# Kernel tuning notes

Measured on AMD Instinct MI355X. Metric: run time of the kernel, lower is better.

The kernel has to match this reference:

```python
import jax, jax.numpy as jnp
import numpy as np

N_NODES = 50000
N_EDGES = 800000
F_IN = 512
HID = 128
OUT = 20


def setup_inputs() -> dict:
    key = jax.random.key(0)
    k1, k2, k3, k4, k5 = jax.random.split(key, 5)
    x = jax.random.normal(k1, (N_NODES, F_IN), dtype=jnp.float32)
    edge_index = jax.random.randint(k2, (2, N_EDGES), 0, N_NODES, dtype=jnp.int64)
    edge_weight = jax.random.uniform(k3, (N_EDGES,), dtype=jnp.float32)
    W1 = jax.random.normal(k4, (F_IN, HID), dtype=jnp.float32) * 0.05
    b1 = jnp.zeros((HID,), dtype=jnp.float32)
    W2 = jax.random.normal(k5, (HID, OUT), dtype=jnp.float32) * 0.05
    b2 = jnp.zeros((OUT,), dtype=jnp.float32)
    return {"x": x, "edge_index": edge_index, "edge_weight": edge_weight,
            "W1": W1, "b1": b1, "W2": W2, "b2": b2}


def _gcn_norm(edge_index, edge_weight, num_nodes):
    # PyG gcn_norm: add self-loops (weight 1), symmetric D^-1/2 (A+I) D^-1/2
    row, col = edge_index[0], edge_index[1]
    loop = jnp.arange(num_nodes, dtype=row.dtype)
    row = jnp.concatenate([row, loop])
    col = jnp.concatenate([col, loop])
    w = jnp.concatenate([edge_weight, jnp.ones((num_nodes,), edge_weight.dtype)])
    deg = jax.ops.segment_sum(w, col, num_segments=num_nodes)
    dinv = jnp.where(deg > 0, jax.lax.rsqrt(deg), 0.0)
    norm = dinv[row] * w * dinv[col]
    return row, col, norm


def _gcn_conv(x, W, b, row, col, norm, num_nodes):
    # linear first (in >= out), then gather-scale-scatter aggregation
    h = x @ W                              # [N, out]
    msg = h[row] * norm[:, None]           # [E+N, out]
    out = jax.ops.segment_sum(msg, col, num_segments=num_nodes)
    return out + b


def reference(x, edge_index, edge_weight, W1, b1, W2, b2):
    n = x.shape[0]
    row, col, norm = _gcn_norm(edge_index, edge_weight, n)
    h = jax.nn.relu(_gcn_conv(x, W1, b1, row, col, norm, n))
    # dropout p=0.6 is identity in eval mode
    out = _gcn_conv(h, W2, b2, row, col, norm, n)
    return out
```

## Files before the change

### kernel.cpp

```cpp
#include <hip/hip_runtime.h>

#define N_NODES 50000
#define N_EDGES 800000
#define F_IN    512
#define HID     128
#define OUT_F   20
#define CAP     48

#define BM  32
#define GEMM_BLOCKS ((N_NODES + BM - 1) / BM)
#define FB_BLOCKS   521
#define FAT_BLOCKS  (FB_BLOCKS * 4)

typedef __bf16 bf16x8 __attribute__((ext_vector_type(8)));
typedef float  f32x4  __attribute__((ext_vector_type(4)));


__global__ void k_prep(const float* __restrict__ W1, __bf16* __restrict__ w1p,
                       int* __restrict__ cursor) {
    int gidx = blockIdx.x * blockDim.x + threadIdx.x;
    if (gidx < F_IN * HID) {
        int k  = gidx >> 7;
        int cc = gidx & (HID - 1);
        int kk = k >> 5;
        int r  = k & 31;
        int g  = (r & 15) >> 2;
        int j  = (r & 3) + ((r >> 4) << 2);
        w1p[((((size_t)kk * 4 + g) * 128 + cc) << 3) + j] = (__bf16)W1[gidx];
    }
    if (gidx < N_NODES) cursor[gidx] = gidx * CAP;
}


__global__ __launch_bounds__(256) void k_fat(const float* __restrict__ x,
                                             const __bf16* __restrict__ w1p,
                                             __bf16* __restrict__ hb,
                                             const int* __restrict__ row,
                                             const int* __restrict__ col,
                                             const float* __restrict__ ew,
                                             int* __restrict__ cursor,
                                             uint2* __restrict__ packed) {
    __shared__ float As[2][BM * 64];
    const int tid = threadIdx.x;
    const int q   = blockIdx.x >> 2;
    const int r3  = blockIdx.x & 3;

    if (r3 == 3) {
        for (int v = q * 256 + tid; v < N_EDGES / 4; v += FB_BLOCKS * 256) {
            int4   c4 = ((const int4*)col)[v];
            int4   r4 = ((const int4*)row)[v];
            float4 w4 = ((const float4*)ew)[v];
            int p0 = atomicAdd(&cursor[c4.x], 1);
            int p1 = atomicAdd(&cursor[c4.y], 1);
            int p2 = atomicAdd(&cursor[c4.z], 1);
            int p3 = atomicAdd(&cursor[c4.w], 1);
            packed[p0] = make_uint2((unsigned)r4.x, __float_as_uint(w4.x));
            packed[p1] = make_uint2((unsigned)r4.y, __float_as_uint(w4.y));
            packed[p2] = make_uint2((unsigned)r4.z, __float_as_uint(w4.z));
            packed[p3] = make_uint2((unsigned)r4.w, __float_as_uint(w4.w));
        }
        return;
    }

    const int gemm_id = q * 3 + r3;
    const int lane = tid & 63;
    const int wid  = tid >> 6;
    const int wm   = wid >> 1;
    const int wn   = wid & 1;
    const int r0   = gemm_id * BM;
    const int g    = lane >> 4;
    const int l15  = lane & 15;

    const __bf16* pb = w1p + (((size_t)g * 128) + wn * 64 + l15) * 8;

    f32x4 acc0 = {}, acc1 = {}, acc2 = {}, acc3 = {};

    auto stage = [&](int buf, int k0) {
#pragma unroll
        for (int i = 0; i < 2; ++i) {
            int cb = wid * 64 + i * 256;
            int c  = cb + lane;
            int rowc = c >> 4;
            int s    = c & 15;
            int gr = r0 + rowc;
            if (gr >= N_NODES) gr = N_NODES - 1;
            const float* src = x + (size_t)gr * F_IN + k0 + ((s ^ (rowc & 7)) << 2);
            __builtin_amdgcn_global_load_lds(
                (const __attribute__((address_space(1))) void*)src,
                (__attribute__((address_space(3))) void*)(&As[buf][(size_t)cb * 4]),
                16, 0, 0);
        }
    };

    const int rowm = wm * 16 + l15;
    const int rbase = rowm * 64;
    const int rx = rowm & 7;

    stage(0, 0);
    __syncthreads();

#pragma unroll
    for (int t = 0; t < 8; ++t) {
        const int buf = t & 1;
        if (t < 7) stage(buf ^ 1, (t + 1) * 64);
#pragma unroll
        for (int kk = 0; kk < 2; ++kk) {
            int slo = ((kk * 8 + g)     ^ rx) << 2;
            int shi = ((kk * 8 + g + 4) ^ rx) << 2;
            f32x4 lo = *(const f32x4*)&As[buf][rbase + slo];
            f32x4 hi = *(const f32x4*)&As[buf][rbase + shi];
            union { __bf16 h[8]; bf16x8 v; } u;
            u.h[0] = (__bf16)lo[0]; u.h[1] = (__bf16)lo[1];
            u.h[2] = (__bf16)lo[2]; u.h[3] = (__bf16)lo[3];
            u.h[4] = (__bf16)hi[0]; u.h[5] = (__bf16)hi[1];
            u.h[6] = (__bf16)hi[2]; u.h[7] = (__bf16)hi[3];
            const __bf16* bp = pb + (size_t)(t * 2 + kk) * 4096;
            bf16x8 b0 = *(const bf16x8*)(bp);
            bf16x8 b1 = *(const bf16x8*)(bp + 128);
            bf16x8 b2 = *(const bf16x8*)(bp + 256);
            bf16x8 b3 = *(const bf16x8*)(bp + 384);
            acc0 = __builtin_amdgcn_mfma_f32_16x16x32_bf16(u.v, b0, acc0, 0, 0, 0);
            acc1 = __builtin_amdgcn_mfma_f32_16x16x32_bf16(u.v, b1, acc1, 0, 0, 0);
            acc2 = __builtin_amdgcn_mfma_f32_16x16x32_bf16(u.v, b2, acc2, 0, 0, 0);
            acc3 = __builtin_amdgcn_mfma_f32_16x16x32_bf16(u.v, b3, acc3, 0, 0, 0);
        }
        __syncthreads();
    }

    const int rb = r0 + wm * 16 + (g << 2);
#pragma unroll
    for (int rr = 0; rr < 4; ++rr) {
        int gr = rb + rr;
        if (gr < N_NODES) {
            __bf16* ho = hb + (size_t)gr * HID + wn * 64 + l15;
            ho[0]  = (__bf16)acc0[rr];
            ho[16] = (__bf16)acc1[rr];
            ho[32] = (__bf16)acc2[rr];
            ho[48] = (__bf16)acc3[rr];
        }
    }
}


__global__ void k_degdinv(const int* __restrict__ cursor, const uint2* __restrict__ packed,
                          int* __restrict__ cnt, float* __restrict__ dinv) {
    int i = blockIdx.x * blockDim.x + threadIdx.x;
    if (i < N_NODES) {
        int n = cursor[i] - i * CAP;
        cnt[i] = n;
        const uint2* seg = packed + (size_t)i * CAP;
        float d = 1.0f;
        for (int k = 0; k < n; ++k) d += __uint_as_float(seg[k].y);
        dinv[i] = rsqrtf(d);
    }
}


__device__ inline float blo(unsigned v) { union { unsigned u; float f; } c; c.u = v << 16; return c.f; }
__device__ inline float bhi(unsigned v) { union { unsigned u; float f; } c; c.u = v & 0xffff0000u; return c.f; }

__global__ __launch_bounds__(128) void k_agg1(const uint2* __restrict__ packed,
                                              const int* __restrict__ cnt,
                                              const __bf16* __restrict__ hb,
                                              const float* __restrict__ dinv,
                                              const float* __restrict__ b1,
                                              unsigned* __restrict__ h1b) {
    __shared__ int   sr[2][64];
    __shared__ float sn[2][64];
    const int w    = threadIdx.x >> 6;
    const int lane = threadIdx.x & 63;
    const int c    = blockIdx.x * 2 + w;
    const unsigned* hbu = (const unsigned*)hb;

    float dic = dinv[c];
    unsigned sv = hbu[((size_t)c << 6) + lane];
    float a0 = dic * dic * blo(sv);
    float a1 = dic * dic * bhi(sv);
    int n = cnt[c];
    const uint2* seg = packed + (size_t)c * CAP;
    for (int base = 0; base < n; base += 64) {
        int m = n - base; if (m > 64) m = 64;
        if (lane < m) {
            uint2 pv = seg[base + lane];
            sr[w][lane] = (int)pv.x;
            sn[w][lane] = __uint_as_float(pv.y) * dinv[pv.x] * dic;
        }
        for (int t = 0; t < m; ++t) {
            float nm = sn[w][t];
            unsigned v = hbu[((size_t)sr[w][t] << 6) + lane];
            a0 = fmaf(nm, blo(v), a0);
            a1 = fmaf(nm, bhi(v), a1);
        }
    }
    float2 bb = *(const float2*)(b1 + 2 * lane);
    a0 += bb.x; a1 += bb.y;
    union { __bf16 h[2]; unsigned u; } o;
    o.h[0] = (__bf16)(a0 > 0.f ? a0 : 0.f);
    o.h[1] = (__bf16)(a1 > 0.f ? a1 : 0.f);
    h1b[((size_t)c << 6) + lane] = o.u;
}


__global__ __launch_bounds__(256) void k_gemm2(const unsigned* __restrict__ h1b,
                                               const float* __restrict__ W2,
                                               float* __restrict__ h2) {
    int g = blockIdx.x * blockDim.x + threadIdx.x;
    int i = g >> 5;
    int j = g & 31;
    if (i >= N_NODES || j >= OUT_F) return;
    float acc = 0.f;
    const unsigned* hr = h1b + ((size_t)i << 6);
    for (int k2 = 0; k2 < 64; ++k2) {
        unsigned v = hr[k2];
        acc = fmaf(blo(v), W2[(2 * k2) * OUT_F + j],
              fmaf(bhi(v), W2[(2 * k2 + 1) * OUT_F + j], acc));
    }
    h2[(size_t)i * OUT_F + j] = acc;
}


__global__ __launch_bounds__(256) void k_agg2(const uint2* __restrict__ packed,
                                              const int* __restrict__ cnt,
                                              const float* __restrict__ h2,
                                              const float* __restrict__ dinv,
                                              const float* __restrict__ b2,
                                              float* __restrict__ out) {
    int g = blockIdx.x * blockDim.x + threadIdx.x;
    int c = g >> 5;
    int j = g & 31;
    if (c >= N_NODES || j >= OUT_F) return;
    float dic = dinv[c];
    float acc = dic * dic * h2[(size_t)c * OUT_F + j] + b2[j];
    int n = cnt[c];
    const uint2* seg = packed + (size_t)c * CAP;
    for (int k = 0; k < n; ++k) {
        uint2 pv = seg[k];
        float nm = __uint_as_float(pv.y) * dinv[pv.x] * dic;
        acc = fmaf(nm, h2[(size_t)pv.x * OUT_F + j], acc);
    }
    out[(size_t)c * OUT_F + j] = acc;
}


extern "C" void kernel_launch(void* const* d_in, const int* in_sizes, int n_in,
                              void* d_out, int out_size, void* d_ws, size_t ws_size,
                              hipStream_t stream) {
    const float* x  = (const float*)d_in[0];
    const int*   ei = (const int*)d_in[1];
    const float* ew = (const float*)d_in[2];
    const float* W1 = (const float*)d_in[3];
    const float* b1 = (const float*)d_in[4];
    const float* W2 = (const float*)d_in[5];
    const float* b2 = (const float*)d_in[6];
    float* out = (float*)d_out;

    const int* row = ei;
    const int* col = ei + N_EDGES;

    char* p = (char*)d_ws;
    float* dinv    = (float*)p;    p += (size_t)N_NODES * 4;
    unsigned* h1b  = (unsigned*)p; p += (size_t)N_NODES * 64 * 4;
    float* h2      = (float*)p;    p += (size_t)N_NODES * OUT_F * 4;
    __bf16* hb     = (__bf16*)p;   p += (size_t)N_NODES * HID * 2;
    __bf16* w1p    = (__bf16*)p;   p += (size_t)F_IN * HID * 2;
    int* cursor    = (int*)p;      p += (size_t)N_NODES * 4;
    int* cnt       = (int*)p;      p += (size_t)N_NODES * 4;
    uint2* packed  = (uint2*)p;    p += (size_t)N_NODES * CAP * 8;

    k_prep<<<(F_IN * HID + 255) / 256, 256, 0, stream>>>(W1, w1p, cursor);

    k_fat<<<FAT_BLOCKS, 256, 0, stream>>>(x, w1p, hb, row, col, ew, cursor, packed);

    k_degdinv<<<(N_NODES + 255) / 256, 256, 0, stream>>>(cursor, packed, cnt, dinv);
    k_agg1<<<N_NODES / 2, 128, 0, stream>>>(packed, cnt, hb, dinv, b1, h1b);

    k_gemm2<<<(N_NODES * 32 + 255) / 256, 256, 0, stream>>>(h1b, W2, h2);
    k_agg2<<<(N_NODES * 32 + 255) / 256, 256, 0, stream>>>(packed, cnt, h2, dinv, b2, out);
}
```

Before: 189.3 us.

## Fuse layer-2 GEMM into layer-1 aggregation and cache edge norms

The second linear layer (128->20) is now computed inside the first aggregation kernel from the fp32 hidden row held in shared memory. Three 20-lane groups each take a slice of K and their partial sums are reduced with shuffles. This removes the h1 bf16 round trip through global memory and one kernel launch. The first aggregation also writes the computed per-edge norm back into the packed edge list, so the second aggregation skips the dinv gather. In exchange, h1 is no longer rounded to bf16 before the second GEMM, and the first aggregation does extra serial FMA work and extra edge writes.

```diff
diff --git a/kernel.cpp b/kernel.cpp
--- a/kernel.cpp
+++ b/kernel.cpp
@@ -159,14 +159,16 @@
 __device__ inline float blo(unsigned v) { union { unsigned u; float f; } c; c.u = v << 16; return c.f; }
 __device__ inline float bhi(unsigned v) { union { unsigned u; float f; } c; c.u = v & 0xffff0000u; return c.f; }
 
-__global__ __launch_bounds__(128) void k_agg1(const uint2* __restrict__ packed,
-                                              const int* __restrict__ cnt,
-                                              const __bf16* __restrict__ hb,
-                                              const float* __restrict__ dinv,
-                                              const float* __restrict__ b1,
-                                              unsigned* __restrict__ h1b) {
+__global__ __launch_bounds__(128) void k_agg1g2(uint2* __restrict__ packed,
+                                                const int* __restrict__ cnt,
+                                                const __bf16* __restrict__ hb,
+                                                const float* __restrict__ dinv,
+                                                const float* __restrict__ b1,
+                                                const float* __restrict__ W2,
+                                                float* __restrict__ h2) {
     __shared__ int   sr[2][64];
     __shared__ float sn[2][64];
+    __shared__ float sh1[2][128];
     const int w    = threadIdx.x >> 6;
     const int lane = threadIdx.x & 63;
     const int c    = blockIdx.x * 2 + w;
@@ -177,13 +179,15 @@
     float a0 = dic * dic * blo(sv);
     float a1 = dic * dic * bhi(sv);
     int n = cnt[c];
-    const uint2* seg = packed + (size_t)c * CAP;
+    uint2* seg = packed + (size_t)c * CAP;
     for (int base = 0; base < n; base += 64) {
         int m = n - base; if (m > 64) m = 64;
         if (lane < m) {
             uint2 pv = seg[base + lane];
+            float nm = __uint_as_float(pv.y) * dinv[pv.x] * dic;
             sr[w][lane] = (int)pv.x;
-            sn[w][lane] = __uint_as_float(pv.y) * dinv[pv.x] * dic;
+            sn[w][lane] = nm;
+            seg[base + lane] = make_uint2(pv.x, __float_as_uint(nm));
         }
         for (int t = 0; t < m; ++t) {
             float nm = sn[w][t];
@@ -194,28 +198,22 @@
     }
     float2 bb = *(const float2*)(b1 + 2 * lane);
     a0 += bb.x; a1 += bb.y;
-    union { __bf16 h[2]; unsigned u; } o;
-    o.h[0] = (__bf16)(a0 > 0.f ? a0 : 0.f);
-    o.h[1] = (__bf16)(a1 > 0.f ? a1 : 0.f);
-    h1b[((size_t)c << 6) + lane] = o.u;
-}
-
-
-__global__ __launch_bounds__(256) void k_gemm2(const unsigned* __restrict__ h1b,
-                                               const float* __restrict__ W2,
-                                               float* __restrict__ h2) {
-    int g = blockIdx.x * blockDim.x + threadIdx.x;
-    int i = g >> 5;
-    int j = g & 31;
-    if (i >= N_NODES || j >= OUT_F) return;
-    float acc = 0.f;
-    const unsigned* hr = h1b + ((size_t)i << 6);
-    for (int k2 = 0; k2 < 64; ++k2) {
-        unsigned v = hr[k2];
-        acc = fmaf(blo(v), W2[(2 * k2) * OUT_F + j],
-              fmaf(bhi(v), W2[(2 * k2 + 1) * OUT_F + j], acc));
-    }
-    h2[(size_t)i * OUT_F + j] = acc;
+    sh1[w][2 * lane]     = a0 > 0.f ? a0 : 0.f;
+    sh1[w][2 * lane + 1] = a1 > 0.f ? a1 : 0.f;
+
+    const int part = lane / 20;
+    const int j    = lane - part * 20;
+    float s = 0.f;
+    if (part < 3) {
+        const int kbeg = part * 43;
+        const int kend = (part == 2) ? 128 : kbeg + 43;
+#pragma unroll 4
+        for (int k = kbeg; k < kend; ++k)
+            s = fmaf(sh1[w][k], W2[k * OUT_F + j], s);
+    }
+    float s1 = __shfl(s, lane + 20);
+    float s2 = __shfl(s, lane + 40);
+    if (lane < 20) h2[(size_t)c * OUT_F + lane] = s + s1 + s2;
 }
 
 
@@ -235,8 +233,7 @@
     const uint2* seg = packed + (size_t)c * CAP;
     for (int k = 0; k < n; ++k) {
         uint2 pv = seg[k];
-        float nm = __uint_as_float(pv.y) * dinv[pv.x] * dic;
-        acc = fmaf(nm, h2[(size_t)pv.x * OUT_F + j], acc);
+        acc = fmaf(__uint_as_float(pv.y), h2[(size_t)pv.x * OUT_F + j], acc);
     }
     out[(size_t)c * OUT_F + j] = acc;
 }
@@ -259,7 +256,6 @@
 
     char* p = (char*)d_ws;
     float* dinv    = (float*)p;    p += (size_t)N_NODES * 4;
-    unsigned* h1b  = (unsigned*)p; p += (size_t)N_NODES * 64 * 4;
     float* h2      = (float*)p;    p += (size_t)N_NODES * OUT_F * 4;
     __bf16* hb     = (__bf16*)p;   p += (size_t)N_NODES * HID * 2;
     __bf16* w1p    = (__bf16*)p;   p += (size_t)F_IN * HID * 2;
@@ -272,8 +268,8 @@
     k_fat<<<FAT_BLOCKS, 256, 0, stream>>>(x, w1p, hb, row, col, ew, cursor, packed);
 
     k_degdinv<<<(N_NODES + 255) / 256, 256, 0, stream>>>(cursor, packed, cnt, dinv);
-    k_agg1<<<N_NODES / 2, 128, 0, stream>>>(packed, cnt, hb, dinv, b1, h1b);
-
-    k_gemm2<<<(N_NODES * 32 + 255) / 256, 256, 0, stream>>>(h1b, W2, h2);
+
+    k_agg1g2<<<N_NODES / 2, 128, 0, stream>>>(packed, cnt, hb, dinv, b1, W2, h2);
+
     k_agg2<<<(N_NODES * 32 + 255) / 256, 256, 0, stream>>>(packed, cnt, h2, dinv, b2, out);
 }
```

Result: faster. 174.6 us (-7.8%).
